# Kernel optimization log

Measured on AMD Instinct MI355X. Metric: run time of the kernel, lower is better.

## Reference

```python
import jax, jax.numpy as jnp
import numpy as np

B, T, L, E = 4, 256, 128, 64  # batch, sample_size (frames), num_harmonies, embedding_size


def setup_inputs() -> dict:
    key = jax.random.key(0)
    k1, k2 = jax.random.split(key)
    return {
        "note_embedding": jax.random.normal(k1, (B, T, E), dtype=jnp.float32),
        "harmony_embedding": jax.random.normal(k2, (B, L, E), dtype=jnp.float32),
    }


def reference(note_embedding, harmony_embedding):
    """SegmentScore.forward: for every segment [s, e] (s <= e), attend the harmony
    embeddings (queries, [B,L,E]) over the note embeddings in that segment
    (keys/values) with scaled dot-product softmax, then score = <harmony, attended>.
    Equivalent closed form: score[b,s,e,l] =
        sum_{t=s..e} softmax_t(raw[b,l,s:e+1])[t] * dot[b,l,t]
    where dot = <harmony_l, note_t> and raw = dot / sqrt(E).
    Vectorized via cumulative sums over the end index for each start index.
    Output: [B, T, T, L]; entries with e < s are 0 (matching torch zeros init).
    """
    scale = 1.0 / jnp.sqrt(jnp.asarray(E, note_embedding.dtype))
    dot = jnp.einsum("ble,bte->blt", harmony_embedding, note_embedding)  # [B,L,T]
    raw = dot * scale
    t_idx = jnp.arange(T)

    def body(carry, s):
        valid = t_idx >= s                                  # [T]
        masked = jnp.where(valid, raw, -jnp.inf)            # [B,L,T]
        m = jnp.max(masked, axis=-1, keepdims=True)         # stable softmax max over t>=s
        exps = jnp.exp(masked - m)                          # 0 where invalid
        denom = jnp.cumsum(exps, axis=-1)                   # running normalizer over e
        numer = jnp.cumsum(exps * dot, axis=-1)             # running <harmony, attended>
        row = jnp.where(valid, numer / jnp.maximum(denom, 1e-30), 0.0)  # [B,L,T_e]
        return carry, row

    _, rows = jax.lax.scan(body, None, t_idx)               # [T_s, B, L, T_e]
    return jnp.transpose(rows, (1, 0, 3, 2))                # [B, T_s, T_e, L]
```

## Files before the change

kernel.cpp:

```cpp
#include <hip/hip_runtime.h>

#define BB 4
#define TT 256
#define LL 128
#define EE 64
#define SCALE 0.125f

typedef float f4v __attribute__((ext_vector_type(4)));

__device__ __forceinline__ void store_nt(float* p, float4 v) {
    __builtin_nontemporal_store(*(f4v*)&v, (f4v*)p);
}

__global__ __launch_bounds__(256) void k_prefix(const float* __restrict__ note,
                                                const float* __restrict__ harm,
                                                double2* __restrict__ P) {
    int b = blockIdx.x >> 7;
    int l = blockIdx.x & 127;
    int t = threadIdx.x;
    int lane = t & 63;
    int wave = t >> 6;

    __shared__ __align__(16) float h[EE];
    if (t < EE) h[t] = harm[(b * LL + l) * EE + t];
    __syncthreads();

    const float4* n4 = (const float4*)(note + (b * TT + t) * EE);
    const float4* h4 = (const float4*)h;
    float acc = 0.f;
#pragma unroll
    for (int i = 0; i < EE / 4; ++i) {
        float4 nv = n4[i];
        float4 hv = h4[i];
        acc += nv.x * hv.x + nv.y * hv.y + nv.z * hv.z + nv.w * hv.w;
    }
    float dot = acc;
    float raw = dot * SCALE;

    float m = raw;
#pragma unroll
    for (int off = 32; off > 0; off >>= 1) m = fmaxf(m, __shfl_xor(m, off));
    __shared__ float wmax[4];
    if (lane == 0) wmax[wave] = m;
    __syncthreads();
    float M = fmaxf(fmaxf(wmax[0], wmax[1]), fmaxf(wmax[2], wmax[3]));

    float ex = __expf(raw - M);
    double vd = (double)ex;
    double vn = (double)ex * (double)dot;

#pragma unroll
    for (int off = 1; off < 64; off <<= 1) {
        double od = __shfl_up(vd, off);
        double on = __shfl_up(vn, off);
        if (lane >= off) { vd += od; vn += on; }
    }
    __shared__ double wtd[4], wtn[4];
    if (lane == 63) { wtd[wave] = vd; wtn[wave] = vn; }
    __syncthreads();
    double od = 0.0, on = 0.0;
#pragma unroll
    for (int w = 0; w < 3; ++w) {
        if (w < wave) { od += wtd[w]; on += wtn[w]; }
    }
    vd += od;
    vn += on;

    P[(b * TT + t) * LL + l] = make_double2(vd, vn);
}

__global__ __launch_bounds__(256) void k_out(const double2* __restrict__ P,
                                             float* __restrict__ out) {
    int blk = blockIdx.x;
    int eq = blk & 3;
    int st = (blk >> 2) & 63;
    int b  = blk >> 8;
    int lq = threadIdx.x & 31;
    int eo = threadIdx.x >> 5;
    int s0 = st * 4;
    int l0 = lq * 4;
    int e_base = eq * 64;

    float* obase = out + ((size_t)(b * TT + s0) * TT) * LL + l0;
    const int srow = TT * LL;

    if (e_base + 63 < s0) {
        float4 z = make_float4(0.f, 0.f, 0.f, 0.f);
#pragma unroll
        for (int it = 0; it < 8; ++it) {
            int e = e_base + it * 8 + eo;
#pragma unroll
            for (int k = 0; k < 4; ++k)
                store_nt(obase + k * srow + e * LL, z);
        }
        return;
    }

    double Psx[4][4], Psy[4][4];
#pragma unroll
    for (int k = 0; k < 4; ++k) {
        int s = s0 + k;
        if (s > 0) {
            const double2* ps = P + (b * TT + s - 1) * LL + l0;
#pragma unroll
            for (int j = 0; j < 4; ++j) {
                double2 v = ps[j];
                Psx[k][j] = v.x;
                Psy[k][j] = v.y;
            }
        } else {
#pragma unroll
            for (int j = 0; j < 4; ++j) { Psx[k][j] = 0.0; Psy[k][j] = 0.0; }
        }
    }

    const double2* pbase = P + b * TT * LL + l0;

    if (e_base >= s0 + 3) {
#pragma unroll 4
        for (int it = 0; it < 8; ++it) {
            int e = e_base + it * 8 + eo;
            const double2* pe = pbase + e * LL;
            double2 Pe[4];
#pragma unroll
            for (int j = 0; j < 4; ++j) Pe[j] = pe[j];

#pragma unroll
            for (int k = 0; k < 4; ++k) {
                float4 r;
                float* rp = (float*)&r;
#pragma unroll
                for (int j = 0; j < 4; ++j) {
                    float den = (float)(Pe[j].x - Psx[k][j]);
                    float num = (float)(Pe[j].y - Psy[k][j]);
                    rp[j] = __fdividef(num, fmaxf(den, 1e-30f));
                }
                store_nt(obase + k * srow + e * LL, r);
            }
        }
        return;
    }

#pragma unroll 2
    for (int it = 0; it < 8; ++it) {
        int e = e_base + it * 8 + eo;
        const double2* pe = pbase + e * LL;
        double2 Pe[4];
#pragma unroll
        for (int j = 0; j < 4; ++j) Pe[j] = pe[j];

#pragma unroll
        for (int k = 0; k < 4; ++k) {
            float4 r;
            float* rp = (float*)&r;
#pragma unroll
            for (int j = 0; j < 4; ++j) {
                float v = 0.f;
                if (e >= s0 + k) {
                    float den = (float)(Pe[j].x - Psx[k][j]);
                    float num = (float)(Pe[j].y - Psy[k][j]);
                    v = __fdividef(num, fmaxf(den, 1e-30f));
                }
                rp[j] = v;
            }
            store_nt(obase + k * srow + e * LL, r);
        }
    }
}

extern "C" void kernel_launch(void* const* d_in, const int* in_sizes, int n_in,
                              void* d_out, int out_size, void* d_ws, size_t ws_size,
                              hipStream_t stream) {
    const float* note = (const float*)d_in[0];
    const float* harm = (const float*)d_in[1];
    float* out = (float*)d_out;

    double2* P = (double2*)d_ws;

    k_prefix<<<BB * LL, 256, 0, stream>>>(note, harm, P);
    k_out<<<BB * 64 * 4, 256, 0, stream>>>(P, out);
}
```

Measured before the change: 155.5 us.

## Split zero-fill into per-row contiguous blocks and launch only non-empty compute tiles

```diff
diff --git a/kernel.cpp b/kernel.cpp
--- a/kernel.cpp
+++ b/kernel.cpp
@@ -69,32 +69,36 @@
     P[(b * TT + t) * LL + l] = make_double2(vd, vn);
 }
 
-__global__ __launch_bounds__(256) void k_out(const double2* __restrict__ P,
-                                             float* __restrict__ out) {
+__global__ __launch_bounds__(256) void k_out2(const double2* __restrict__ P,
+                                              float* __restrict__ out) {
     int blk = blockIdx.x;
-    int eq = blk & 3;
-    int st = (blk >> 2) & 63;
-    int b  = blk >> 8;
+    const int srow = TT * LL;
+
+    if (blk >= 640) {
+        int idx = blk - 640;
+        int b = idx >> 8;
+        int s = idx & 255;
+        float* base = out + ((size_t)(b * TT + s) * TT) * LL;
+        int n4 = s * (LL / 4);
+        float4 z = make_float4(0.f, 0.f, 0.f, 0.f);
+        for (int i = threadIdx.x; i < n4; i += 256)
+            store_nt(base + 4 * i, z);
+        return;
+    }
+
+    int b = blk / 160;
+    int r = blk - b * 160;
+    int eq, st;
+    if (r < 16)      { eq = 0; st = r; }
+    else if (r < 48) { eq = 1; st = r - 16; }
+    else if (r < 96) { eq = 2; st = r - 48; }
+    else             { eq = 3; st = r - 96; }
+
     int lq = threadIdx.x & 31;
     int eo = threadIdx.x >> 5;
     int s0 = st * 4;
     int l0 = lq * 4;
     int e_base = eq * 64;
-
-    float* obase = out + ((size_t)(b * TT + s0) * TT) * LL + l0;
-    const int srow = TT * LL;
-
-    if (e_base + 63 < s0) {
-        float4 z = make_float4(0.f, 0.f, 0.f, 0.f);
-#pragma unroll
-        for (int it = 0; it < 8; ++it) {
-            int e = e_base + it * 8 + eo;
-#pragma unroll
-            for (int k = 0; k < 4; ++k)
-                store_nt(obase + k * srow + e * LL, z);
-        }
-        return;
-    }
 
     double Psx[4][4], Psy[4][4];
 #pragma unroll
@@ -115,6 +119,7 @@
     }
 
     const double2* pbase = P + b * TT * LL + l0;
+    float* obase = out + ((size_t)(b * TT + s0) * TT) * LL + l0;
 
     if (e_base >= s0 + 3) {
 #pragma unroll 4
@@ -127,15 +132,15 @@
 
 #pragma unroll
             for (int k = 0; k < 4; ++k) {
-                float4 r;
-                float* rp = (float*)&r;
+                float4 rv;
+                float* rp = (float*)&rv;
 #pragma unroll
                 for (int j = 0; j < 4; ++j) {
                     float den = (float)(Pe[j].x - Psx[k][j]);
                     float num = (float)(Pe[j].y - Psy[k][j]);
                     rp[j] = __fdividef(num, fmaxf(den, 1e-30f));
                 }
-                store_nt(obase + k * srow + e * LL, r);
+                store_nt(obase + k * srow + e * LL, rv);
             }
         }
         return;
@@ -151,19 +156,17 @@
 
 #pragma unroll
         for (int k = 0; k < 4; ++k) {
-            float4 r;
-            float* rp = (float*)&r;
+            if (e >= s0 + k) {
+                float4 rv;
+                float* rp = (float*)&rv;
 #pragma unroll
-            for (int j = 0; j < 4; ++j) {
-                float v = 0.f;
-                if (e >= s0 + k) {
+                for (int j = 0; j < 4; ++j) {
                     float den = (float)(Pe[j].x - Psx[k][j]);
                     float num = (float)(Pe[j].y - Psy[k][j]);
-                    v = __fdividef(num, fmaxf(den, 1e-30f));
+                    rp[j] = __fdividef(num, fmaxf(den, 1e-30f));
                 }
-                rp[j] = v;
+                store_nt(obase + k * srow + e * LL, rv);
             }
-            store_nt(obase + k * srow + e * LL, r);
         }
     }
 }
@@ -178,5 +181,5 @@
     double2* P = (double2*)d_ws;
 
     k_prefix<<<BB * LL, 256, 0, stream>>>(note, harm, P);
-    k_out<<<BB * 64 * 4, 256, 0, stream>>>(P, out);
+    k_out2<<<640 + BB * TT, 256, 0, stream>>>(P, out);
 }
```

Result: slower. 161.1 us (+3.6%).
